# Performance work log

Hardware: AMD Instinct MI355X
Metric: run time of the kernel (lower is better)

Reference implementation:

```python
import jax, jax.numpy as jnp
import numpy as np

N, NA, LAYERS = 8, 4, 4
NTOT = N + NA
DIM = 2 ** NTOT
B = 1024

# Diagonal of the fixed CZ brick layer (CZ is diagonal, so one elementwise pass per layer).
# Qubit 0 is the most-significant bit of the state index (tensorcircuit convention).
def _cz_diag():
    idx = np.arange(DIM)
    bits = (idx[None, :] >> (NTOT - 1 - np.arange(NTOT)[:, None])) & 1  # [NTOT, DIM]
    par = np.zeros(DIM, dtype=np.int64)
    for i in range(NTOT // 2):
        par += bits[2 * i] * bits[2 * i + 1]
    for i in range((NTOT - 1) // 2):
        par += bits[2 * i + 1] * bits[2 * i + 2]
    return jnp.asarray(1.0 - 2.0 * (par % 2), dtype=jnp.complex64)

CZ_DIAG = _cz_diag()

def _apply_1q(state, U, q):
    # state: [B, DIM]; apply 2x2 unitary U on qubit q (batched over samples)
    l, r = 2 ** q, 2 ** (NTOT - q - 1)
    s = state.reshape(-1, l, 2, r)
    return jnp.einsum('ij,bljr->blir', U, s).reshape(-1, DIM)

def _back_circuit(state, params):
    # hardware-efficient ansatz: per layer RX,RY on every qubit, then CZ bricks
    for lay in range(LAYERS):
        off = 2 * NTOT * lay
        for q in range(NTOT):
            th = params[off + q] * 0.5
            c = jnp.cos(th).astype(jnp.complex64)
            ms = (-1j) * jnp.sin(th).astype(jnp.complex64)
            Rx = jnp.stack([jnp.stack([c, ms]), jnp.stack([ms, c])])
            state = _apply_1q(state, Rx, q)
            th = params[off + NTOT + q] * 0.5
            c, s = jnp.cos(th), jnp.sin(th)
            Ry = jnp.stack([jnp.stack([c, -s]), jnp.stack([s, c])]).astype(jnp.complex64)
            state = _apply_1q(state, Ry, q)
        state = state * CZ_DIAG
    return state

def setup_inputs() -> dict:
    key = jax.random.key(0)
    k1, k2, k3, k4 = jax.random.split(key, 4)
    return {
        'inputs_re': jax.random.normal(k1, (B, DIM), jnp.float32),
        'inputs_im': jax.random.normal(k2, (B, DIM), jnp.float32),
        'params': jax.random.normal(k3, (2 * NTOT * LAYERS,), jnp.float32),
        'u': jax.random.uniform(k4, (B,), jnp.float32),
    }

def reference(inputs_re, inputs_im, params, u):
    state = (inputs_re + 1j * inputs_im).astype(jnp.complex64)
    full = _back_circuit(state, params)                      # [B, 2^n_tot]
    s3 = full.reshape(B, 2 ** NA, 2 ** N)                    # [B, 2^na, 2^n]
    probs = jnp.sum(s3.real ** 2 + s3.imag ** 2, axis=2)     # ancilla outcome probs
    cdf = jnp.cumsum(probs, axis=1)
    thresh = u * cdf[:, -1]                                  # inverse-CDF multinomial
    m = jnp.argmax(cdf >= thresh[:, None], axis=1)           # [B] sampled outcome
    post = s3[jnp.arange(B), m]                              # [B, 2^n] collapsed state
    norm = jnp.sqrt(jnp.sum(post.real ** 2 + post.imag ** 2, axis=1, keepdims=True))
    post = post / norm
    return jnp.stack([post.real, post.imag], axis=-1)        # [B, 2^n, 2]
```

## Files before the change

kernel.cpp:

```cpp
#include <hip/hip_runtime.h>
#include <math.h>

#define NTOT   12
#define DIM    4096
#define LAYERS 4
#define NB     1024
#define SPAD   4608

typedef float v2f __attribute__((ext_vector_type(2)));

template<int G>
__device__ __forceinline__ void gate_pk(v2f (&x)[16], v2f P1, v2f P2) {
#pragma unroll
    for (int p = 0; p < 8; ++p) {
        const int j0 = ((p >> G) << (G + 1)) | (p & ((1 << G) - 1));
        const int j1 = j0 | (1 << G);
        const v2f x0 = x[j0], x1 = x[j1];
        v2f t, u;
        asm("v_pk_mul_f32 %0, %1, %2 op_sel:[1,1] op_sel_hi:[1,0] neg_hi:[1,0]"
            : "=v"(t) : "v"(P2), "v"(x1));
        asm("v_pk_fma_f32 %0, %1, %2, %0 op_sel:[1,0,0] op_sel_hi:[1,1,1] neg_lo:[1,0,0] neg_hi:[1,0,0]"
            : "+v"(t) : "v"(P1), "v"(x1));
        asm("v_pk_fma_f32 %0, %1, %2, %0 op_sel:[0,1,0] op_sel_hi:[0,0,1] neg_lo:[1,0,0]"
            : "+v"(t) : "v"(P2), "v"(x0));
        asm("v_pk_fma_f32 %0, %1, %2, %0 op_sel:[0,0,0] op_sel_hi:[0,1,1]"
            : "+v"(t) : "v"(P1), "v"(x0));
        asm("v_pk_mul_f32 %0, %1, %2 op_sel:[0,1] op_sel_hi:[0,0] neg_hi:[1,0]"
            : "=v"(u) : "v"(P2), "v"(x1));
        asm("v_pk_fma_f32 %0, %1, %2, %0 op_sel:[0,0,0] op_sel_hi:[0,1,1]"
            : "+v"(u) : "v"(P1), "v"(x1));
        asm("v_pk_fma_f32 %0, %1, %2, %0 op_sel:[1,1,0] op_sel_hi:[1,0,1] neg_hi:[1,0,0]"
            : "+v"(u) : "v"(P2), "v"(x0));
        asm("v_pk_fma_f32 %0, %1, %2, %0 op_sel:[1,0,0] op_sel_hi:[1,1,1]"
            : "+v"(u) : "v"(P1), "v"(x0));
        x[j0] = t; x[j1] = u;
    }
}

__device__ __forceinline__ void apply4(v2f (&x)[16], const float4* gco, int base) {
    float4 c;
    c = gco[base + 3]; gate_pk<0>(x, (v2f){c.x, c.y}, (v2f){c.z, c.w});
    c = gco[base + 2]; gate_pk<1>(x, (v2f){c.x, c.y}, (v2f){c.z, c.w});
    c = gco[base + 1]; gate_pk<2>(x, (v2f){c.x, c.y}, (v2f){c.z, c.w});
    c = gco[base + 0]; gate_pk<3>(x, (v2f){c.x, c.y}, (v2f){c.z, c.w});
}

__device__ __forceinline__ void applyCZ(v2f (&x)[16], const int (&sw)[16]) {
#pragma unroll
    for (int j = 0; j < 16; ++j) {
        x[j].x = __uint_as_float(__float_as_uint(x[j].x) ^ sw[j]);
        x[j].y = __uint_as_float(__float_as_uint(x[j].y) ^ sw[j]);
    }
}

__global__ __launch_bounds__(256, 4) void qddpm_kernel(
    const float* __restrict__ in_re,
    const float* __restrict__ in_im,
    const float* __restrict__ params,
    const float* __restrict__ uu,
    float* __restrict__ out)
{
    __shared__ v2f    S[SPAD];
    __shared__ float4 gco[48];
    __shared__ float  sprob[16];

    const int b = blockIdx.x;
    const int t = threadIdx.x;
    const float uval = uu[b];

    const int baseA = t + 2 * (t >> 4);
    const int baseB = (t >> 4) * 288 + (t & 15);
    const int baseC = t * 18;

    v2f x[16];

    {
        const float4* re4 = (const float4*)(in_re + (size_t)b * DIM + t * 16);
        const float4* im4 = (const float4*)(in_im + (size_t)b * DIM + t * 16);
#pragma unroll
        for (int q = 0; q < 4; ++q) {
            const float4 vr = re4[q];
            const float4 vi = im4[q];
            x[4 * q + 0] = (v2f){vr.x, vi.x};
            x[4 * q + 1] = (v2f){vr.y, vi.y};
            x[4 * q + 2] = (v2f){vr.z, vi.z};
            x[4 * q + 3] = (v2f){vr.w, vi.w};
        }
    }

    {
        const int lg = t & 63;
        if (lg < 48) {
            const int lay = lg / 12, q = lg - lay * 12;
            float c1, s1, c2, s2;
            sincosf(params[lay * 24 + q] * 0.5f, &s1, &c1);
            sincosf(params[lay * 24 + 12 + q] * 0.5f, &s2, &c2);
            gco[lg] = make_float4(c1 * c2, c1 * s2, s1 * s2, s1 * c2);
        }
    }

    int swA[16], swC[16];
#pragma unroll
    for (int j = 0; j < 16; ++j) {
        const int iC = t * 16 + j;
        swC[j] = (__popc(iC & (iC >> 1) & 0x7FF) & 1) << 31;
        const int iA = j * 256 + t;
        swA[j] = (__popc(iA & (iA >> 1) & 0x7FF) & 1) << 31;
    }

    apply4(x, gco, 0 * 12 + 8);
    {
        float4* dst = (float4*)(S + baseC);
#pragma unroll
        for (int q = 0; q < 8; ++q)
            dst[q] = make_float4(x[2 * q].x, x[2 * q].y, x[2 * q + 1].x, x[2 * q + 1].y);
    }

#pragma unroll
    for (int j = 0; j < 16; ++j) x[j] = S[baseB + 18 * j];
    apply4(x, gco, 0 * 12 + 4);
#pragma unroll
    for (int j = 0; j < 16; ++j) S[baseB + 18 * j] = x[j];
    __syncthreads();

#pragma unroll
    for (int j = 0; j < 16; ++j) x[j] = S[baseA + 288 * j];
    apply4(x, gco, 0 * 12 + 0);
    applyCZ(x, swA);
    apply4(x, gco, 1 * 12 + 0);
#pragma unroll
    for (int j = 0; j < 16; ++j) S[baseA + 288 * j] = x[j];
    __syncthreads();

#pragma unroll
    for (int j = 0; j < 16; ++j) x[j] = S[baseB + 18 * j];
    apply4(x, gco, 1 * 12 + 4);
#pragma unroll
    for (int j = 0; j < 16; ++j) S[baseB + 18 * j] = x[j];

    {
        const float4* src = (const float4*)(S + baseC);
#pragma unroll
        for (int q = 0; q < 8; ++q) {
            const float4 v = src[q];
            x[2 * q]     = (v2f){v.x, v.y};
            x[2 * q + 1] = (v2f){v.z, v.w};
        }
    }
    apply4(x, gco, 1 * 12 + 8);
    applyCZ(x, swC);
    apply4(x, gco, 2 * 12 + 8);
    {
        float4* dst = (float4*)(S + baseC);
#pragma unroll
        for (int q = 0; q < 8; ++q)
            dst[q] = make_float4(x[2 * q].x, x[2 * q].y, x[2 * q + 1].x, x[2 * q + 1].y);
    }

#pragma unroll
    for (int j = 0; j < 16; ++j) x[j] = S[baseB + 18 * j];
    apply4(x, gco, 2 * 12 + 4);
#pragma unroll
    for (int j = 0; j < 16; ++j) S[baseB + 18 * j] = x[j];
    __syncthreads();

#pragma unroll
    for (int j = 0; j < 16; ++j) x[j] = S[baseA + 288 * j];
    apply4(x, gco, 2 * 12 + 0);
    applyCZ(x, swA);
    apply4(x, gco, 3 * 12 + 0);
#pragma unroll
    for (int j = 0; j < 16; ++j) S[baseA + 288 * j] = x[j];
    __syncthreads();

#pragma unroll
    for (int j = 0; j < 16; ++j) x[j] = S[baseB + 18 * j];
    apply4(x, gco, 3 * 12 + 4);
#pragma unroll
    for (int j = 0; j < 16; ++j) S[baseB + 18 * j] = x[j];

    {
        const float4* src = (const float4*)(S + baseC);
#pragma unroll
        for (int q = 0; q < 8; ++q) {
            const float4 v = src[q];
            x[2 * q]     = (v2f){v.x, v.y};
            x[2 * q + 1] = (v2f){v.z, v.w};
        }
    }
    apply4(x, gco, 3 * 12 + 8);
    applyCZ(x, swC);
    {
        v2f acc2 = (v2f){0.0f, 0.0f};
#pragma unroll
        for (int j = 0; j < 16; ++j) acc2 += x[j] * x[j];
        float4* dst = (float4*)(S + baseC);
#pragma unroll
        for (int q = 0; q < 8; ++q)
            dst[q] = make_float4(x[2 * q].x, x[2 * q].y, x[2 * q + 1].x, x[2 * q + 1].y);
        float partial = acc2.x + acc2.y;
#pragma unroll
        for (int o = 8; o > 0; o >>= 1)
            partial += __shfl_down(partial, o, 16);
        if ((t & 15) == 0) sprob[t >> 4] = partial;
    }
    __syncthreads();

    {
        float cdf[16];
        float a = 0.0f;
#pragma unroll
        for (int i = 0; i < 16; ++i) { a += sprob[i]; cdf[i] = a; }
        const float thresh = uval * a;
        int m = 0;
#pragma unroll
        for (int i = 15; i >= 0; --i) { if (cdf[i] >= thresh) m = i; }
        const float rn = 1.0f / sqrtf(sprob[m]);
        const v2f amp = S[baseA + 288 * m];
        ((float2*)out)[(size_t)b * 256 + t] = make_float2(amp.x * rn, amp.y * rn);
    }
}

extern "C" void kernel_launch(void* const* d_in, const int* in_sizes, int n_in,
                              void* d_out, int out_size, void* d_ws, size_t ws_size,
                              hipStream_t stream) {
    const float* in_re  = (const float*)d_in[0];
    const float* in_im  = (const float*)d_in[1];
    const float* params = (const float*)d_in[2];
    const float* u      = (const float*)d_in[3];
    float* out = (float*)d_out;
    qddpm_kernel<<<NB, 256, 0, stream>>>(in_re, in_im, params, u, out);
}
```

Measured before the change: 108.8 us.

## Process two batch samples per block with interleaved state vectors

Each block now simulates two samples instead of one, holding two register state vectors and two shared-memory buffers, and launches half as many blocks. Gate coefficient setup, CZ sign masks and barriers are shared across the two samples, and the interleaved work gives the scheduler more independent instructions between syncs. In exchange, register and LDS use per block doubles (launch bounds lowered to 2), which cuts occupancy and may cause spills.

```diff
diff --git a/kernel.cpp b/kernel.cpp
--- a/kernel.cpp
+++ b/kernel.cpp
@@ -1,7 +1,6 @@
 #include <hip/hip_runtime.h>
 #include <math.h>
 
-#define NTOT   12
 #define DIM    4096
 #define LAYERS 4
 #define NB     1024
@@ -53,50 +52,107 @@
     }
 }
 
-__global__ __launch_bounds__(256, 4) void qddpm_kernel(
+__device__ __forceinline__ void loadA(v2f (&x)[16], const v2f* Sp, int baseA) {
+#pragma unroll
+    for (int j = 0; j < 16; ++j) x[j] = Sp[baseA + 288 * j];
+}
+__device__ __forceinline__ void storeA(const v2f (&x)[16], v2f* Sp, int baseA) {
+#pragma unroll
+    for (int j = 0; j < 16; ++j) Sp[baseA + 288 * j] = x[j];
+}
+__device__ __forceinline__ void loadB(v2f (&x)[16], const v2f* Sp, int baseB) {
+#pragma unroll
+    for (int j = 0; j < 16; ++j) x[j] = Sp[baseB + 18 * j];
+}
+__device__ __forceinline__ void storeB(const v2f (&x)[16], v2f* Sp, int baseB) {
+#pragma unroll
+    for (int j = 0; j < 16; ++j) Sp[baseB + 18 * j] = x[j];
+}
+__device__ __forceinline__ void loadC(v2f (&x)[16], const v2f* Sp, int baseC) {
+    const float4* src = (const float4*)(Sp + baseC);
+#pragma unroll
+    for (int q = 0; q < 8; ++q) {
+        const float4 v = src[q];
+        x[2 * q]     = (v2f){v.x, v.y};
+        x[2 * q + 1] = (v2f){v.z, v.w};
+    }
+}
+__device__ __forceinline__ void storeC(const v2f (&x)[16], v2f* Sp, int baseC) {
+    float4* dst = (float4*)(Sp + baseC);
+#pragma unroll
+    for (int q = 0; q < 8; ++q)
+        dst[q] = make_float4(x[2 * q].x, x[2 * q].y, x[2 * q + 1].x, x[2 * q + 1].y);
+}
+__device__ __forceinline__ void gloadC(v2f (&x)[16], const float* re, const float* im) {
+    const float4* re4 = (const float4*)re;
+    const float4* im4 = (const float4*)im;
+#pragma unroll
+    for (int q = 0; q < 4; ++q) {
+        const float4 vr = re4[q];
+        const float4 vi = im4[q];
+        x[4 * q + 0] = (v2f){vr.x, vi.x};
+        x[4 * q + 1] = (v2f){vr.y, vi.y};
+        x[4 * q + 2] = (v2f){vr.z, vi.z};
+        x[4 * q + 3] = (v2f){vr.w, vi.w};
+    }
+}
+__device__ __forceinline__ void probs16(const v2f (&x)[16], float* spr, int t) {
+    v2f a2 = (v2f){0.0f, 0.0f};
+#pragma unroll
+    for (int j = 0; j < 16; ++j) a2 += x[j] * x[j];
+    float p = a2.x + a2.y;
+#pragma unroll
+    for (int o = 8; o > 0; o >>= 1) p += __shfl_down(p, o, 16);
+    if ((t & 15) == 0) spr[t >> 4] = p;
+}
+__device__ __forceinline__ void emit(const v2f* Sp, const float* spr, float uval,
+                                     float2* o2, int t, int baseA) {
+    float cdf[16];
+    float a = 0.0f;
+#pragma unroll
+    for (int i = 0; i < 16; ++i) { a += spr[i]; cdf[i] = a; }
+    const float th = uval * a;
+    int m = 0;
+#pragma unroll
+    for (int i = 15; i >= 0; --i) { if (cdf[i] >= th) m = i; }
+    const float rn = 1.0f / sqrtf(spr[m]);
+    const v2f amp = Sp[baseA + 288 * m];
+    o2[t] = make_float2(amp.x * rn, amp.y * rn);
+}
+
+__global__ __launch_bounds__(256, 2) void qddpm_kernel(
     const float* __restrict__ in_re,
     const float* __restrict__ in_im,
     const float* __restrict__ params,
     const float* __restrict__ uu,
     float* __restrict__ out)
 {
-    __shared__ v2f    S[SPAD];
+    __shared__ v2f    S0[SPAD], S1[SPAD];
     __shared__ float4 gco[48];
-    __shared__ float  sprob[16];
+    __shared__ float  sprob[2][16];
 
     const int b = blockIdx.x;
     const int t = threadIdx.x;
-    const float uval = uu[b];
+    const int l = t & 63;
+    const float u0 = uu[2 * b], u1 = uu[2 * b + 1];
 
     const int baseA = t + 2 * (t >> 4);
     const int baseB = (t >> 4) * 288 + (t & 15);
     const int baseC = t * 18;
 
-    v2f x[16];
-
-    {
-        const float4* re4 = (const float4*)(in_re + (size_t)b * DIM + t * 16);
-        const float4* im4 = (const float4*)(in_im + (size_t)b * DIM + t * 16);
-#pragma unroll
-        for (int q = 0; q < 4; ++q) {
-            const float4 vr = re4[q];
-            const float4 vi = im4[q];
-            x[4 * q + 0] = (v2f){vr.x, vi.x};
-            x[4 * q + 1] = (v2f){vr.y, vi.y};
-            x[4 * q + 2] = (v2f){vr.z, vi.z};
-            x[4 * q + 3] = (v2f){vr.w, vi.w};
-        }
-    }
-
-    {
-        const int lg = t & 63;
-        if (lg < 48) {
-            const int lay = lg / 12, q = lg - lay * 12;
-            float c1, s1, c2, s2;
-            sincosf(params[lay * 24 + q] * 0.5f, &s1, &c1);
-            sincosf(params[lay * 24 + 12 + q] * 0.5f, &s2, &c2);
-            gco[lg] = make_float4(c1 * c2, c1 * s2, s1 * s2, s1 * c2);
-        }
+    v2f x[16], y[16];
+
+    gloadC(x, in_re + (size_t)(2 * b) * DIM + t * 16,
+              in_im + (size_t)(2 * b) * DIM + t * 16);
+    gloadC(y, in_re + (size_t)(2 * b + 1) * DIM + t * 16,
+              in_im + (size_t)(2 * b + 1) * DIM + t * 16);
+
+    if (l < 48) {
+        const int lay = l / 12, q = l - lay * 12;
+        float c1, s1, c2, s2;
+        sincosf(params[lay * 24 + q] * 0.5f, &s1, &c1);
+        sincosf(params[lay * 24 + 12 + q] * 0.5f, &s2, &c2);
+        gco[l] = make_float4(c1 * c2, c1 * s2, s1 * s2, s1 * c2);
     }
 
     int swA[16], swC[16];
@@ -108,117 +164,49 @@
         swA[j] = (__popc(iA & (iA >> 1) & 0x7FF) & 1) << 31;
     }
 
-    apply4(x, gco, 0 * 12 + 8);
-    {
-        float4* dst = (float4*)(S + baseC);
-#pragma unroll
-        for (int q = 0; q < 8; ++q)
-            dst[q] = make_float4(x[2 * q].x, x[2 * q].y, x[2 * q + 1].x, x[2 * q + 1].y);
-    }
-
-#pragma unroll
-    for (int j = 0; j < 16; ++j) x[j] = S[baseB + 18 * j];
-    apply4(x, gco, 0 * 12 + 4);
-#pragma unroll
-    for (int j = 0; j < 16; ++j) S[baseB + 18 * j] = x[j];
-    __syncthreads();
-
-#pragma unroll
-    for (int j = 0; j < 16; ++j) x[j] = S[baseA + 288 * j];
-    apply4(x, gco, 0 * 12 + 0);
-    applyCZ(x, swA);
-    apply4(x, gco, 1 * 12 + 0);
-#pragma unroll
-    for (int j = 0; j < 16; ++j) S[baseA + 288 * j] = x[j];
-    __syncthreads();
-
-#pragma unroll
-    for (int j = 0; j < 16; ++j) x[j] = S[baseB + 18 * j];
-    apply4(x, gco, 1 * 12 + 4);
-#pragma unroll
-    for (int j = 0; j < 16; ++j) S[baseB + 18 * j] = x[j];
-
-    {
-        const float4* src = (const float4*)(S + baseC);
-#pragma unroll
-        for (int q = 0; q < 8; ++q) {
-            const float4 v = src[q];
-            x[2 * q]     = (v2f){v.x, v.y};
-            x[2 * q + 1] = (v2f){v.z, v.w};
-        }
-    }
-    apply4(x, gco, 1 * 12 + 8);
-    applyCZ(x, swC);
-    apply4(x, gco, 2 * 12 + 8);
-    {
-        float4* dst = (float4*)(S + baseC);
-#pragma unroll
-        for (int q = 0; q < 8; ++q)
-            dst[q] = make_float4(x[2 * q].x, x[2 * q].y, x[2 * q + 1].x, x[2 * q + 1].y);
-    }
-
-#pragma unroll
-    for (int j = 0; j < 16; ++j) x[j] = S[baseB + 18 * j];
-    apply4(x, gco, 2 * 12 + 4);
-#pragma unroll
-    for (int j = 0; j < 16; ++j) S[baseB + 18 * j] = x[j];
-    __syncthreads();
-
-#pragma unroll
-    for (int j = 0; j < 16; ++j) x[j] = S[baseA + 288 * j];
-    apply4(x, gco, 2 * 12 + 0);
-    applyCZ(x, swA);
-    apply4(x, gco, 3 * 12 + 0);
-#pragma unroll
-    for (int j = 0; j < 16; ++j) S[baseA + 288 * j] = x[j];
-    __syncthreads();
-
-#pragma unroll
-    for (int j = 0; j < 16; ++j) x[j] = S[baseB + 18 * j];
-    apply4(x, gco, 3 * 12 + 4);
-#pragma unroll
-    for (int j = 0; j < 16; ++j) S[baseB + 18 * j] = x[j];
-
-    {
-        const float4* src = (const float4*)(S + baseC);
-#pragma unroll
-        for (int q = 0; q < 8; ++q) {
-            const float4 v = src[q];
-            x[2 * q]     = (v2f){v.x, v.y};
-            x[2 * q + 1] = (v2f){v.z, v.w};
-        }
-    }
-    apply4(x, gco, 3 * 12 + 8);
-    applyCZ(x, swC);
-    {
-        v2f acc2 = (v2f){0.0f, 0.0f};
-#pragma unroll
-        for (int j = 0; j < 16; ++j) acc2 += x[j] * x[j];
-        float4* dst = (float4*)(S + baseC);
-#pragma unroll
-        for (int q = 0; q < 8; ++q)
-            dst[q] = make_float4(x[2 * q].x, x[2 * q].y, x[2 * q + 1].x, x[2 * q + 1].y);
-        float partial = acc2.x + acc2.y;
-#pragma unroll
-        for (int o = 8; o > 0; o >>= 1)
-            partial += __shfl_down(partial, o, 16);
-        if ((t & 15) == 0) sprob[t >> 4] = partial;
-    }
-    __syncthreads();
-
-    {
-        float cdf[16];
-        float a = 0.0f;
-#pragma unroll
-        for (int i = 0; i < 16; ++i) { a += sprob[i]; cdf[i] = a; }
-        const float thresh = uval * a;
-        int m = 0;
-#pragma unroll
-        for (int i = 15; i >= 0; --i) { if (cdf[i] >= thresh) m = i; }
-        const float rn = 1.0f / sqrtf(sprob[m]);
-        const v2f amp = S[baseA + 288 * m];
-        ((float2*)out)[(size_t)b * 256 + t] = make_float2(amp.x * rn, amp.y * rn);
-    }
+    apply4(x, gco, 8);  storeC(x, S0, baseC);
+    apply4(y, gco, 8);  storeC(y, S1, baseC);
+    loadB(x, S0, baseB); apply4(x, gco, 4);  storeB(x, S0, baseB);
+    loadB(y, S1, baseB); apply4(y, gco, 4);  storeB(y, S1, baseB);
+    __syncthreads();
+
+    loadA(x, S0, baseA); loadA(y, S1, baseA);
+    apply4(x, gco, 0);  applyCZ(x, swA); apply4(x, gco, 12); storeA(x, S0, baseA);
+    apply4(y, gco, 0);  applyCZ(y, swA); apply4(y, gco, 12); storeA(y, S1, baseA);
+    __syncthreads();
+
+    loadB(x, S0, baseB); loadB(y, S1, baseB);
+    apply4(x, gco, 16); storeB(x, S0, baseB);
+    apply4(y, gco, 16); storeB(y, S1, baseB);
+    loadC(x, S0, baseC);
+    apply4(x, gco, 20); applyCZ(x, swC); apply4(x, gco, 32); storeC(x, S0, baseC);
+    loadC(y, S1, baseC);
+    apply4(y, gco, 20); applyCZ(y, swC); apply4(y, gco, 32); storeC(y, S1, baseC);
+    loadB(x, S0, baseB); apply4(x, gco, 28); storeB(x, S0, baseB);
+    loadB(y, S1, baseB); apply4(y, gco, 28); storeB(y, S1, baseB);
+    __syncthreads();
+
+    loadA(x, S0, baseA); loadA(y, S1, baseA);
+    apply4(x, gco, 24); applyCZ(x, swA); apply4(x, gco, 36); storeA(x, S0, baseA);
+    apply4(y, gco, 24); applyCZ(y, swA); apply4(y, gco, 36); storeA(y, S1, baseA);
+    __syncthreads();
+
+    loadB(x, S0, baseB); loadB(y, S1, baseB);
+    apply4(x, gco, 40); storeB(x, S0, baseB);
+    apply4(y, gco, 40); storeB(y, S1, baseB);
+    loadC(x, S0, baseC);
+    apply4(x, gco, 44); applyCZ(x, swC);
+    probs16(x, sprob[0], t);
+    storeC(x, S0, baseC);
+    loadC(y, S1, baseC);
+    apply4(y, gco, 44); applyCZ(y, swC);
+    probs16(y, sprob[1], t);
+    storeC(y, S1, baseC);
+    __syncthreads();
+
+    float2* o2 = (float2*)out;
+    emit(S0, sprob[0], u0, o2 + (size_t)(2 * b) * 256,     t, baseA);
+    emit(S1, sprob[1], u1, o2 + (size_t)(2 * b + 1) * 256, t, baseA);
 }
 
 extern "C" void kernel_launch(void* const* d_in, const int* in_sizes, int n_in,
@@ -229,5 +217,5 @@
     const float* params = (const float*)d_in[2];
     const float* u      = (const float*)d_in[3];
     float* out = (float*)d_out;
-    qddpm_kernel<<<NB, 256, 0, stream>>>(in_re, in_im, params, u, out);
-}
+    qddpm_kernel<<<NB / 2, 256, 0, stream>>>(in_re, in_im, params, u, out);
+}
```

Result: slower. 111.5 us (+2.5%).
